# Optimization experiments

Measured on AMD Instinct MI355X. Metric: run time of the kernel, lower is better.

Reference implementation:

```python
import jax, jax.numpy as jnp
import numpy as np

B = 2048
SEQ_LEN = 512; PRED_LEN = 336; PATCH_LEN = 16; STRIDE = 8; CHANNELS = 16
D_MODEL = 128; HIDDEN = 256; PRUNE = 64
NUM_PATCHES = (SEQ_LEN - PATCH_LEN) // STRIDE + 1        # 63
TARGET_PATCHES = (PRED_LEN - 1) // STRIDE + 1            # 42 Euler steps


def setup_inputs() -> dict:
    key = jax.random.key(0)
    ks = jax.random.split(key, 12)
    w = lambda k, shape: (jax.random.normal(k, shape, jnp.float32) * 0.05)
    PC = PATCH_LEN * CHANNELS
    return {
        "x": jax.random.normal(ks[0], (B, SEQ_LEN, CHANNELS), jnp.float32),
        "W_pe": w(ks[1], (D_MODEL, PC)), "b_pe": jnp.zeros((D_MODEL,), jnp.float32),
        "W_conv": w(ks[2], (D_MODEL, 1, 3)), "b_conv": jnp.zeros((D_MODEL,), jnp.float32),
        "W_cmp": w(ks[3], (PRUNE, D_MODEL * NUM_PATCHES)), "b_cmp": jnp.zeros((PRUNE,), jnp.float32),
        "W_n1": w(ks[4], (HIDDEN, PRUNE)), "b_n1": jnp.zeros((HIDDEN,), jnp.float32),
        "W_n2": w(ks[5], (PRUNE, HIDDEN)), "b_n2": jnp.zeros((PRUNE,), jnp.float32),
        "W_l1": w(ks[6], (HIDDEN, PRUNE)), "b_l1": jnp.zeros((HIDDEN,), jnp.float32),
        "W_l2": w(ks[7], (D_MODEL, HIDDEN)), "b_l2": jnp.zeros((D_MODEL,), jnp.float32),
        "span_A": jnp.asarray(0.5, jnp.float32),
        "W_d1": w(ks[8], (PC, D_MODEL)), "b_d1": jnp.zeros((PC,), jnp.float32),
        "W_d2": w(ks[9], (PC, PC)), "b_d2": jnp.zeros((PC,), jnp.float32),
    }


def reference(x, W_pe, b_pe, W_conv, b_conv, W_cmp, b_cmp,
              W_n1, b_n1, W_n2, b_n2, W_l1, b_l1, W_l2, b_l2,
              span_A, W_d1, b_d1, W_d2, b_d2):
    silu = jax.nn.silu
    Bsz, L, C = x.shape

    # --- PatchEmbedding: unfold + rearrange 'b c n p -> b n (c p)' + Linear ---
    pidx = (jnp.arange(NUM_PATCHES) * STRIDE)[:, None] + jnp.arange(PATCH_LEN)[None, :]  # (N, P)
    patches = x[:, pidx, :]                                  # (B, N, P, C)
    patches = jnp.transpose(patches, (0, 1, 3, 2)).reshape(Bsz, NUM_PATCHES, C * PATCH_LEN)
    pe = patches @ W_pe.T + b_pe                             # (B, N, D)

    # --- depthwise Conv1d(k=3, padding=2, groups=D), SiLU, truncate to N ---
    feat = jnp.transpose(pe, (0, 2, 1))                      # (B, D, N)
    conv = jax.lax.conv_general_dilated(
        feat, W_conv, window_strides=(1,), padding=[(2, 2)],
        dimension_numbers=('NCH', 'OIH', 'NCH'), feature_group_count=D_MODEL)
    feat = silu(conv + b_conv[None, :, None])[:, :, :NUM_PATCHES]
    patch_flat = jnp.transpose(feat, (0, 2, 1)).reshape(Bsz, -1)   # (B, N*D)

    a0 = patch_flat @ W_cmp.T + b_cmp                        # (B, PRUNE); dropout = eval identity
    z0 = pe[:, -1, :]                                        # (B, D)

    # tspan built from float(span_A * K) in torch -> detached; dt = clamp(span_A)
    dt = jax.lax.stop_gradient(jnp.clip(span_A, 1e-8, 5.0))

    # circulant gather index: circ[b, i, j] = c[b, (j - i) % D]
    roll_idx = (jnp.arange(D_MODEL)[None, :] - jnp.arange(D_MODEL)[:, None]) % D_MODEL

    def euler_step(s, _):
        a = s[:, :PRUNE]
        z = s[:, PRUNE:]
        da = jnp.tanh(silu(a @ W_n1.T + b_n1) @ W_n2.T + b_n2)        # AODEFunc.net
        c = jnp.tanh(silu(a @ W_l1.T + b_l1) @ W_l2.T + b_l2)        # lat2out -> (B, D)
        dz = jnp.einsum('bij,bj->bi', c[:, roll_idx], z)              # circulant @ z
        s_new = s + dt * jnp.concatenate([da, dz], axis=-1)
        return s_new, s_new[:, PRUNE:]

    s0 = jnp.concatenate([a0, z0], axis=-1)
    _, z_traj = jax.lax.scan(euler_step, s0, None, length=TARGET_PATCHES)  # (K, B, D)

    # --- patch decoder (Linear -> SiLU -> Linear; dropout identity) ---
    dec = silu(z_traj @ W_d1.T + b_d1) @ W_d2.T + b_d2       # (K, B, P*C)
    pred_patches = dec.reshape(TARGET_PATCHES, Bsz, PATCH_LEN, C)

    # --- overlap-add reconstruction ---
    pos = (jnp.arange(TARGET_PATCHES) * STRIDE)[:, None] + jnp.arange(PATCH_LEN)[None, :]  # (K, P)
    valid = (pos < PRED_LEN).reshape(-1)
    pos_safe = jnp.where(valid, pos.reshape(-1), PRED_LEN)   # dump OOB into extra bin
    vals = jnp.transpose(pred_patches, (1, 0, 2, 3)).reshape(Bsz, -1, C)
    vals = vals * valid.astype(x.dtype)[None, :, None]
    out = jnp.zeros((Bsz, PRED_LEN + 1, C), x.dtype).at[:, pos_safe, :].add(vals)[:, :PRED_LEN]
    counts = jnp.zeros((PRED_LEN + 1,), x.dtype).at[pos_safe].add(valid.astype(x.dtype))[:PRED_LEN]
    x_pred = out / (counts[None, :, None] + 1e-6)

    return (x, x_pred)
```

## Files before the change

kernel.cpp:

```cpp
#include <hip/hip_runtime.h>
#include <math.h>

#define BATCH 2048
#define SEQ 512
#define CH 16
#define PLEN 16
#define NP 63
#define TP 42
#define DM 128
#define PCDIM 256
#define PRUNE 64
#define HID 256
#define PRED 336

#define O_WPET2   0
#define O_WCMPT4  32768
#define O_W1T4    548864
#define O_W2T4    581632
#define O_WD1T4   647168
#define O_WD2T4   679936
#define O_SSTATE  745472
#define O_FEAT    1138688
#define O_ZTRAJ   17653760
#define WS_TOTAL  28663808

__device__ __forceinline__ float silu_f(float v){ return v / (1.0f + expf(-v)); }

__global__ void repack_kernel(const float* __restrict__ Wpe, const float* __restrict__ Wcmp,
                              const float* __restrict__ Wn1, const float* __restrict__ Wn2,
                              const float* __restrict__ Wl1, const float* __restrict__ Wl2,
                              const float* __restrict__ Wd1, const float* __restrict__ Wd2,
                              float* __restrict__ ws){
  const int tot = 745472;
  for (int e = blockIdx.x*blockDim.x + threadIdx.x; e < tot; e += gridDim.x*blockDim.x){
    float v; int x = e;
    if (x < 32768){
      int kk = x & 3, d = (x>>2)&127, k4 = x>>9;
      v = Wpe[d*256 + k4*4 + kk];
    } else if ((x -= 32768) < 516096){
      int kk = x&3, j = (x>>2)&63, k4 = x>>8;
      v = Wcmp[j*8064 + k4*4 + kk];
    } else if ((x -= 516096) < 32768){
      int kk = x&3, j = (x>>2)&511, k4 = x>>11; int k = k4*4+kk;
      v = (j < 256) ? Wn1[j*64 + k] : Wl1[(j-256)*64 + k];
    } else if ((x -= 32768) < 65536){
      int kk = x&3, j = (x>>2)&255, k4 = x>>10; int k = k4*4+kk;
      v = (j < 64) ? Wn2[j*256 + k] : ((j < 192) ? Wl2[(j-64)*256 + k] : 0.0f);
    } else if ((x -= 65536) < 32768){
      int kk = x&3, j = (x>>2)&255, k4 = x>>10;
      v = Wd1[j*128 + k4*4 + kk];
    } else { x -= 32768;
      int kk = x&3, j = (x>>2)&255, k4 = x>>10;
      v = Wd2[j*256 + k4*4 + kk];
    }
    ws[e] = v;
  }
}

__global__ __launch_bounds__(256) void k1_embed(const float* __restrict__ x,
        const float* __restrict__ ws, const float* __restrict__ b_pe,
        const float* __restrict__ Wconv, const float* __restrict__ b_conv,
        float* __restrict__ feat, float* __restrict__ sstate){
  __shared__ __align__(16) float xT[16*512];
  __shared__ float pe_s[63*132];
  const float* __restrict__ WpeT2 = ws + O_WPET2;
  const int b = blockIdx.x;
  const int t = threadIdx.x;
  const float* xb = x + (size_t)b*(SEQ*CH);
  for (int rep = 0; rep < 2; ++rep){
    int l = t + rep*256;
    const float* src = xb + l*16;
    #pragma unroll
    for (int c4 = 0; c4 < 4; ++c4){
      float4 v = *(const float4*)(src + c4*4);
      xT[(c4*4+0)*512 + l] = v.x;
      xT[(c4*4+1)*512 + l] = v.y;
      xT[(c4*4+2)*512 + l] = v.z;
      xT[(c4*4+3)*512 + l] = v.w;
    }
  }
  __syncthreads();
  const int dgrp = t & 15;
  const int p0 = (t >> 4) * 4;
  float acc[8][4];
  #pragma unroll
  for (int j = 0; j < 8; ++j)
    #pragma unroll
    for (int pi = 0; pi < 4; ++pi) acc[j][pi] = 0.0f;
  for (int c = 0; c < 16; ++c){
    #pragma unroll
    for (int t4 = 0; t4 < 4; ++t4){
      const int k4 = c*4 + t4;
      float4 xv[4];
      #pragma unroll
      for (int pi = 0; pi < 4; ++pi){
        int p = p0 + pi; int pr = (p < 63) ? p : 62;
        xv[pi] = *(const float4*)(&xT[c*512 + pr*8 + t4*4]);
      }
      #pragma unroll
      for (int j = 0; j < 8; ++j){
        float4 wv = *(const float4*)(&WpeT2[(k4*128 + j*16 + dgrp)*4]);
        #pragma unroll
        for (int pi = 0; pi < 4; ++pi){
          acc[j][pi] += wv.x*xv[pi].x + wv.y*xv[pi].y + wv.z*xv[pi].z + wv.w*xv[pi].w;
        }
      }
    }
  }
  #pragma unroll
  for (int j = 0; j < 8; ++j){
    int d = j*16 + dgrp;
    float bp = b_pe[d];
    #pragma unroll
    for (int pi = 0; pi < 4; ++pi){
      int p = p0 + pi;
      if (p < 63) pe_s[p*132 + d] = acc[j][pi] + bp;
    }
  }
  __syncthreads();
  const int d = t & 127;
  const int ph = t >> 7;
  float w0 = Wconv[d*3+0], w1 = Wconv[d*3+1], w2 = Wconv[d*3+2];
  float bc = b_conv[d];
  float* featb = feat + (size_t)b*(NP*DM);
  for (int q = 0; q < 32; ++q){
    int p = ph*32 + q;
    if (p < 63){
      float s = bc + w2*pe_s[p*132+d];
      if (p >= 1) s += w1*pe_s[(p-1)*132+d];
      if (p >= 2) s += w0*pe_s[(p-2)*132+d];
      featb[p*128 + d] = silu_f(s);
    }
  }
  if (ph == 0){
    sstate[(size_t)b*192 + 64 + d] = pe_s[62*132 + d];
  }
}

__global__ __launch_bounds__(256) void k2_cmp(const float* __restrict__ feat,
      const float* __restrict__ ws, const float* __restrict__ b_cmp,
      float* __restrict__ sstate){
  const float* __restrict__ WcmpT4 = ws + O_WCMPT4;
  __shared__ __align__(16) float fs[8*512];
  const int b0 = blockIdx.x * 8;
  const int t = threadIdx.x;
  const int j = t & 63, bq = t >> 6;
  float acc0 = 0.0f, acc1 = 0.0f;
  for (int chk = 0; chk < 16; ++chk){
    const int k0 = chk*512;
    const int lim = (8064 - k0 < 512) ? (8064 - k0) : 512;
    __syncthreads();
    for (int u = 0; u < 16; ++u){
      int idx = u*256 + t;
      int bb = idx >> 9, kk = idx & 511;
      fs[idx] = (kk < lim) ? feat[(size_t)(b0+bb)*8064 + k0 + kk] : 0.0f;
    }
    __syncthreads();
    const int nk4 = lim >> 2;
    const float* wbase = &WcmpT4[(k0>>2)*256 + j*4];
    const float* f0 = &fs[(bq*2+0)*512];
    const float* f1 = &fs[(bq*2+1)*512];
    for (int k4 = 0; k4 < nk4; ++k4){
      float4 wv = *(const float4*)(wbase + k4*256);
      float4 a0 = *(const float4*)(f0 + k4*4);
      float4 a1 = *(const float4*)(f1 + k4*4);
      acc0 += wv.x*a0.x + wv.y*a0.y + wv.z*a0.z + wv.w*a0.w;
      acc1 += wv.x*a1.x + wv.y*a1.y + wv.z*a1.z + wv.w*a1.w;
    }
  }
  float bj = b_cmp[j];
  sstate[(size_t)(b0 + bq*2 + 0)*192 + j] = acc0 + bj;
  sstate[(size_t)(b0 + bq*2 + 1)*192 + j] = acc1 + bj;
}

__global__ __launch_bounds__(512) void k3_ode(const float* __restrict__ ws,
      const float* __restrict__ b_n1, const float* __restrict__ b_l1,
      const float* __restrict__ b_n2, const float* __restrict__ b_l2,
      const float* __restrict__ spanA,
      float* __restrict__ sstate, float* __restrict__ ztraj){
  const float* __restrict__ W1T4 = ws + O_W1T4;
  const float* __restrict__ W2T4 = ws + O_W2T4;
  __shared__ __align__(16) float a_s[8*64];
  __shared__ __align__(16) float h_s[8*512];
  __shared__ __align__(16) float c_s[8*128];
  __shared__ __align__(16) float zd[8*260];
  __shared__ float part2[2*8*256];
  __shared__ __align__(16) float dzp[2*8*128];
  const int t = threadIdx.x;
  const int b0 = blockIdx.x * 8;
  const float dt = fminf(fmaxf(spanA[0], 1e-8f), 5.0f);
  {
    int r = t >> 6, jj = t & 63;
    a_s[t] = sstate[(size_t)(b0+r)*192 + jj];
    for (int u = 0; u < 2; ++u){
      int idx = u*512 + t; int rr = idx >> 7, i = idx & 127;
      float zv = sstate[(size_t)(b0+rr)*192 + 64 + i];
      zd[rr*260 + i] = zv; zd[rr*260 + 128 + i] = zv;
    }
  }
  const float b1 = (t < 256) ? b_n1[t] : b_l1[t-256];
  const int j2 = t & 255;
  const int rb = t >> 8;
  const float bias2 = (j2 < 64) ? b_n2[j2] : ((j2 < 192) ? b_l2[j2-64] : 0.0f);
  __syncthreads();

  for (int st = 0; st < TP; ++st){
    {
      float acc[8];
      #pragma unroll
      for (int r = 0; r < 8; ++r) acc[r] = 0.0f;
      for (int k4 = 0; k4 < 16; ++k4){
        float4 wv = *(const float4*)(&W1T4[(k4*512 + t)*4]);
        #pragma unroll
        for (int r = 0; r < 8; ++r){
          float4 av = *(const float4*)(&a_s[r*64 + k4*4]);
          acc[r] += wv.x*av.x + wv.y*av.y + wv.z*av.z + wv.w*av.w;
        }
      }
      #pragma unroll
      for (int r = 0; r < 8; ++r) h_s[r*512 + t] = silu_f(acc[r] + b1);
    }
    __syncthreads();
    {
      const int kh = t >> 8;
      if (j2 < 192){
        float acc[8];
        #pragma unroll
        for (int r = 0; r < 8; ++r) acc[r] = 0.0f;
        const int hoff = (j2 < 64) ? 0 : 256;
        for (int k4i = 0; k4i < 32; ++k4i){
          const int k4 = kh*32 + k4i;
          float4 wv = *(const float4*)(&W2T4[(k4*256 + j2)*4]);
          #pragma unroll
          for (int r = 0; r < 8; ++r){
            float4 hv = *(const float4*)(&h_s[r*512 + hoff + k4*4]);
            acc[r] += wv.x*hv.x + wv.y*hv.y + wv.z*hv.z + wv.w*hv.w;
          }
        }
        #pragma unroll
        for (int r = 0; r < 8; ++r) part2[(kh*8 + r)*256 + j2] = acc[r];
      }
    }
    __syncthreads();
    if (j2 < 192){
      #pragma unroll
      for (int u = 0; u < 4; ++u){
        int r = u*2 + rb;
        float v = part2[r*256 + j2] + part2[(8+r)*256 + j2] + bias2;
        float tv = tanhf(v);
        if (j2 < 64) a_s[r*64 + j2] += dt * tv;
        else         c_s[r*128 + (j2-64)] = tv;
      }
    }
    __syncthreads();
    {
      const int i0 = (t & 31) * 4;
      const int r  = (t >> 5) & 7;
      const int mh = t >> 8;
      const int mbase = mh * 64;
      float m0=0.f, m1=0.f, m2=0.f, m3=0.f;
      const float* zr = &zd[r*260];
      const float* cr = &c_s[r*128];
      for (int mc = 0; mc < 16; ++mc){
        const int m = mbase + mc*4;
        float4 cv = *(const float4*)(cr + m);
        float4 za = *(const float4*)(zr + i0 + m);
        float4 zb = *(const float4*)(zr + i0 + m + 4);
        m0 += cv.x*za.x + cv.y*za.y + cv.z*za.z + cv.w*za.w;
        m1 += cv.x*za.y + cv.y*za.z + cv.z*za.w + cv.w*zb.x;
        m2 += cv.x*za.z + cv.y*za.w + cv.z*zb.x + cv.w*zb.y;
        m3 += cv.x*za.w + cv.y*zb.x + cv.z*zb.y + cv.w*zb.z;
      }
      *(float4*)(&dzp[(mh*8 + r)*128 + i0]) = make_float4(m0, m1, m2, m3);
    }
    __syncthreads();
    {
      float* zt = ztraj + (size_t)st*(BATCH*DM);
      for (int u = 0; u < 2; ++u){
        int idx = u*512 + t; int r = idx >> 7, i = idx & 127;
        float dz = dzp[r*128 + i] + dzp[(8+r)*128 + i];
        float zn = zd[r*260 + i] + dt*dz;
        zd[r*260 + i] = zn; zd[r*260 + 128 + i] = zn;
        zt[(size_t)(b0+r)*128 + i] = zn;
      }
    }
    __syncthreads();
  }
}

__global__ __launch_bounds__(256) void k4_dec(const float* __restrict__ ztraj,
    const float* __restrict__ ws, const float* __restrict__ b_d1,
    const float* __restrict__ b_d2, float* __restrict__ xpred){
  const float* __restrict__ Wd1T4 = ws + O_WD1T4;
  const float* __restrict__ Wd2T4 = ws + O_WD2T4;
  __shared__ __align__(16) float z_s[32*128];
  __shared__ __align__(16) float h_sh[32*256];
  const int t = threadIdx.x;
  const int m0 = blockIdx.x * 32;
  for (int u = 0; u < 4; ++u){
    int idx4 = u*256 + t;
    ((float4*)z_s)[idx4] = *(const float4*)(ztraj + (size_t)m0*128 + idx4*4);
  }
  __syncthreads();
  float acc[32];
  #pragma unroll
  for (int r = 0; r < 32; ++r) acc[r] = 0.0f;
  for (int k4 = 0; k4 < 32; ++k4){
    float4 wv = *(const float4*)(&Wd1T4[(k4*256 + t)*4]);
    #pragma unroll
    for (int r = 0; r < 32; ++r){
      float4 zv = *(const float4*)(&z_s[r*128 + k4*4]);
      acc[r] += wv.x*zv.x + wv.y*zv.y + wv.z*zv.z + wv.w*zv.w;
    }
  }
  {
    float bd1 = b_d1[t];
    #pragma unroll
    for (int r = 0; r < 32; ++r) h_sh[r*256 + t] = silu_f(acc[r] + bd1);
  }
  __syncthreads();
  #pragma unroll
  for (int r = 0; r < 32; ++r) acc[r] = 0.0f;
  for (int k4 = 0; k4 < 64; ++k4){
    float4 wv = *(const float4*)(&Wd2T4[(k4*256 + t)*4]);
    #pragma unroll
    for (int r = 0; r < 32; ++r){
      float4 hv = *(const float4*)(&h_sh[r*256 + k4*4]);
      acc[r] += wv.x*hv.x + wv.y*hv.y + wv.z*hv.z + wv.w*hv.w;
    }
  }
  const float bd2 = b_d2[t];
  const int tt_ = t >> 4, cc = t & 15;
  #pragma unroll
  for (int r = 0; r < 32; ++r){
    int m = m0 + r;
    int st = m >> 11;
    int b  = m & 2047;
    int tau = st*8 + tt_;
    if (tau < PRED){
      float scale = 1.0f / (((tau < 8) ? 1.0f : 2.0f) + 1e-6f);
      atomicAdd(&xpred[(size_t)b*(PRED*CH) + tau*16 + cc], (acc[r] + bd2) * scale);
    }
  }
}

extern "C" void kernel_launch(void* const* d_in, const int* in_sizes, int n_in,
                              void* d_out, int out_size, void* d_ws, size_t ws_size,
                              hipStream_t stream){
  const float* x    = (const float*)d_in[0];
  const float* Wpe  = (const float*)d_in[1];
  const float* bpe  = (const float*)d_in[2];
  const float* Wconv= (const float*)d_in[3];
  const float* bconv= (const float*)d_in[4];
  const float* Wcmp = (const float*)d_in[5];
  const float* bcmp = (const float*)d_in[6];
  const float* Wn1  = (const float*)d_in[7];
  const float* bn1  = (const float*)d_in[8];
  const float* Wn2  = (const float*)d_in[9];
  const float* bn2  = (const float*)d_in[10];
  const float* Wl1  = (const float*)d_in[11];
  const float* bl1  = (const float*)d_in[12];
  const float* Wl2  = (const float*)d_in[13];
  const float* bl2  = (const float*)d_in[14];
  const float* span = (const float*)d_in[15];
  const float* Wd1  = (const float*)d_in[16];
  const float* bd1  = (const float*)d_in[17];
  const float* Wd2  = (const float*)d_in[18];
  const float* bd2  = (const float*)d_in[19];
  float* out = (float*)d_out;
  float* ws  = (float*)d_ws;

  const size_t XN  = (size_t)BATCH*SEQ*CH;
  const size_t XPN = (size_t)BATCH*PRED*CH;

  hipMemcpyAsync(out, x, XN*sizeof(float), hipMemcpyDeviceToDevice, stream);
  hipMemsetAsync(out + XN, 0, XPN*sizeof(float), stream);

  float* sstate = ws + O_SSTATE;
  float* feat   = ws + O_FEAT;
  float* ztraj  = ws + O_ZTRAJ;

  repack_kernel<<<256, 256, 0, stream>>>(Wpe, Wcmp, Wn1, Wn2, Wl1, Wl2, Wd1, Wd2, ws);
  k1_embed<<<BATCH, 256, 0, stream>>>(x, ws, bpe, Wconv, bconv, feat, sstate);
  k2_cmp<<<BATCH/8, 256, 0, stream>>>(feat, ws, bcmp, sstate);
  k3_ode<<<BATCH/8, 512, 0, stream>>>(ws, bn1, bl1, bn2, bl2, span, sstate, ztraj);
  k4_dec<<<(TP*BATCH)/32, 256, 0, stream>>>(ztraj, ws, bd1, bd2, out + XN);
}
```

Before: 1.779 ms.

## Restructure ODE kernel to 1024 threads with overlapped stages; shrink decoder tiles

The ODE kernel now runs 1024 threads per block. It reorders each Euler step so that the second matmul and the z-update from the previous step run in the same phase, and the next step's first matmul runs alongside the circulant product. This cuts the barriers per step from five to three and splits the reductions four ways. The decoder kernel moves from 32-row to 16-row tiles, with each thread computing two output columns, which lowers register pressure and doubles the number of blocks. SiLU switches to the fast __expf intrinsic, at a small accuracy cost. The larger ODE blocks raise shared-memory and register demand per block, which may reduce occupancy.

```diff
diff --git a/kernel.cpp b/kernel.cpp
--- a/kernel.cpp
+++ b/kernel.cpp
@@ -22,9 +22,8 @@
 #define O_SSTATE  745472
 #define O_FEAT    1138688
 #define O_ZTRAJ   17653760
-#define WS_TOTAL  28663808
-
-__device__ __forceinline__ float silu_f(float v){ return v / (1.0f + expf(-v)); }
+
+__device__ __forceinline__ float silu_f(float v){ return v / (1.0f + __expf(-v)); }
 
 __global__ void repack_kernel(const float* __restrict__ Wpe, const float* __restrict__ Wcmp,
                               const float* __restrict__ Wn1, const float* __restrict__ Wn2,
@@ -173,7 +172,7 @@
   sstate[(size_t)(b0 + bq*2 + 1)*192 + j] = acc1 + bj;
 }
 
-__global__ __launch_bounds__(512) void k3_ode(const float* __restrict__ ws,
+__global__ __launch_bounds__(1024) void k3_ode(const float* __restrict__ ws,
       const float* __restrict__ b_n1, const float* __restrict__ b_l1,
       const float* __restrict__ b_n2, const float* __restrict__ b_l2,
       const float* __restrict__ spanA,
@@ -184,24 +183,51 @@
   __shared__ __align__(16) float h_s[8*512];
   __shared__ __align__(16) float c_s[8*128];
   __shared__ __align__(16) float zd[8*260];
-  __shared__ float part2[2*8*256];
-  __shared__ __align__(16) float dzp[2*8*128];
+  __shared__ __align__(16) float part2[4*8*256];
+  __shared__ __align__(16) float dzp[4*8*128];
   const int t = threadIdx.x;
   const int b0 = blockIdx.x * 8;
   const float dt = fminf(fmaxf(spanA[0], 1e-8f), 5.0f);
-  {
+
+  if (t < 512){
     int r = t >> 6, jj = t & 63;
     a_s[t] = sstate[(size_t)(b0+r)*192 + jj];
-    for (int u = 0; u < 2; ++u){
-      int idx = u*512 + t; int rr = idx >> 7, i = idx & 127;
-      float zv = sstate[(size_t)(b0+rr)*192 + 64 + i];
-      zd[rr*260 + i] = zv; zd[rr*260 + 128 + i] = zv;
-    }
-  }
-  const float b1 = (t < 256) ? b_n1[t] : b_l1[t-256];
+  }
+  {
+    int r = t >> 7, i = t & 127;
+    float zv = sstate[(size_t)(b0+r)*192 + 64 + i];
+    zd[r*260 + i] = zv; zd[r*260 + 128 + i] = zv;
+  }
+  const int jP0 = t & 511;
+  const int rhP0 = t >> 9;
+  const float b1 = (jP0 < 256) ? b_n1[jP0] : b_l1[jP0-256];
+  const int khA = t >> 8;
   const int j2 = t & 255;
-  const int rb = t >> 8;
   const float bias2 = (j2 < 64) ? b_n2[j2] : ((j2 < 192) ? b_l2[j2-64] : 0.0f);
+  const int hoffA = (j2 < 64) ? 0 : 256;
+  const int rrB = t >> 8;
+  const int mhC = t >> 8;
+  const int rC  = (t >> 5) & 7;
+  const int i0C = (t & 31) * 4;
+  const int rZ = t >> 7, iZ = t & 127;
+  __syncthreads();
+
+  {
+    float acc4[4];
+    #pragma unroll
+    for (int q = 0; q < 4; ++q) acc4[q] = 0.0f;
+    for (int k4 = 0; k4 < 16; ++k4){
+      float4 wv = *(const float4*)(&W1T4[(k4*512 + jP0)*4]);
+      #pragma unroll
+      for (int q = 0; q < 4; ++q){
+        float4 av = *(const float4*)(&a_s[(rhP0*4+q)*64 + k4*4]);
+        acc4[q] += wv.x*av.x + wv.y*av.y + wv.z*av.z + wv.w*av.w;
+      }
+    }
+    #pragma unroll
+    for (int q = 0; q < 4; ++q)
+      h_s[(rhP0*4+q)*512 + jP0] = silu_f(acc4[q] + b1);
+  }
   __syncthreads();
 
   for (int st = 0; st < TP; ++st){
@@ -209,82 +235,81 @@
       float acc[8];
       #pragma unroll
       for (int r = 0; r < 8; ++r) acc[r] = 0.0f;
-      for (int k4 = 0; k4 < 16; ++k4){
-        float4 wv = *(const float4*)(&W1T4[(k4*512 + t)*4]);
+      for (int k4i = 0; k4i < 16; ++k4i){
+        const int k4 = khA*16 + k4i;
+        float4 wv = *(const float4*)(&W2T4[(k4*256 + j2)*4]);
         #pragma unroll
         for (int r = 0; r < 8; ++r){
-          float4 av = *(const float4*)(&a_s[r*64 + k4*4]);
-          acc[r] += wv.x*av.x + wv.y*av.y + wv.z*av.z + wv.w*av.w;
+          float4 hv = *(const float4*)(&h_s[r*512 + hoffA + k4*4]);
+          acc[r] += wv.x*hv.x + wv.y*hv.y + wv.z*hv.z + wv.w*hv.w;
         }
       }
       #pragma unroll
-      for (int r = 0; r < 8; ++r) h_s[r*512 + t] = silu_f(acc[r] + b1);
+      for (int r = 0; r < 8; ++r) part2[(khA*8 + r)*256 + j2] = acc[r];
+    }
+    if (st > 0){
+      float dz = dzp[(0*8+rZ)*128 + iZ] + dzp[(1*8+rZ)*128 + iZ]
+               + dzp[(2*8+rZ)*128 + iZ] + dzp[(3*8+rZ)*128 + iZ];
+      float zn = zd[rZ*260 + iZ] + dt*dz;
+      zd[rZ*260 + iZ] = zn; zd[rZ*260 + 128 + iZ] = zn;
+      ztraj[(size_t)(st-1)*(BATCH*DM) + (size_t)(b0+rZ)*128 + iZ] = zn;
     }
     __syncthreads();
-    {
-      const int kh = t >> 8;
-      if (j2 < 192){
-        float acc[8];
-        #pragma unroll
-        for (int r = 0; r < 8; ++r) acc[r] = 0.0f;
-        const int hoff = (j2 < 64) ? 0 : 256;
-        for (int k4i = 0; k4i < 32; ++k4i){
-          const int k4 = kh*32 + k4i;
-          float4 wv = *(const float4*)(&W2T4[(k4*256 + j2)*4]);
-          #pragma unroll
-          for (int r = 0; r < 8; ++r){
-            float4 hv = *(const float4*)(&h_s[r*512 + hoff + k4*4]);
-            acc[r] += wv.x*hv.x + wv.y*hv.y + wv.z*hv.z + wv.w*hv.w;
-          }
-        }
-        #pragma unroll
-        for (int r = 0; r < 8; ++r) part2[(kh*8 + r)*256 + j2] = acc[r];
-      }
-    }
-    __syncthreads();
+
     if (j2 < 192){
       #pragma unroll
-      for (int u = 0; u < 4; ++u){
-        int r = u*2 + rb;
-        float v = part2[r*256 + j2] + part2[(8+r)*256 + j2] + bias2;
+      for (int u = 0; u < 2; ++u){
+        int r = rrB*2 + u;
+        float v = part2[(0*8+r)*256 + j2] + part2[(1*8+r)*256 + j2]
+                + part2[(2*8+r)*256 + j2] + part2[(3*8+r)*256 + j2] + bias2;
         float tv = tanhf(v);
         if (j2 < 64) a_s[r*64 + j2] += dt * tv;
         else         c_s[r*128 + (j2-64)] = tv;
       }
     }
     __syncthreads();
+
     {
-      const int i0 = (t & 31) * 4;
-      const int r  = (t >> 5) & 7;
-      const int mh = t >> 8;
-      const int mbase = mh * 64;
+      float acc4[4];
+      #pragma unroll
+      for (int q = 0; q < 4; ++q) acc4[q] = 0.0f;
+      for (int k4 = 0; k4 < 16; ++k4){
+        float4 wv = *(const float4*)(&W1T4[(k4*512 + jP0)*4]);
+        #pragma unroll
+        for (int q = 0; q < 4; ++q){
+          float4 av = *(const float4*)(&a_s[(rhP0*4+q)*64 + k4*4]);
+          acc4[q] += wv.x*av.x + wv.y*av.y + wv.z*av.z + wv.w*av.w;
+        }
+      }
+      #pragma unroll
+      for (int q = 0; q < 4; ++q)
+        h_s[(rhP0*4+q)*512 + jP0] = silu_f(acc4[q] + b1);
+    }
+    {
       float m0=0.f, m1=0.f, m2=0.f, m3=0.f;
-      const float* zr = &zd[r*260];
-      const float* cr = &c_s[r*128];
-      for (int mc = 0; mc < 16; ++mc){
-        const int m = mbase + mc*4;
+      const float* zr = &zd[rC*260];
+      const float* cr = &c_s[rC*128];
+      #pragma unroll
+      for (int mc = 0; mc < 8; ++mc){
+        const int m = mhC*32 + mc*4;
         float4 cv = *(const float4*)(cr + m);
-        float4 za = *(const float4*)(zr + i0 + m);
-        float4 zb = *(const float4*)(zr + i0 + m + 4);
+        float4 za = *(const float4*)(zr + i0C + m);
+        float4 zb = *(const float4*)(zr + i0C + m + 4);
         m0 += cv.x*za.x + cv.y*za.y + cv.z*za.z + cv.w*za.w;
         m1 += cv.x*za.y + cv.y*za.z + cv.z*za.w + cv.w*zb.x;
         m2 += cv.x*za.z + cv.y*za.w + cv.z*zb.x + cv.w*zb.y;
         m3 += cv.x*za.w + cv.y*zb.x + cv.z*zb.y + cv.w*zb.z;
       }
-      *(float4*)(&dzp[(mh*8 + r)*128 + i0]) = make_float4(m0, m1, m2, m3);
+      *(float4*)(&dzp[(mhC*8 + rC)*128 + i0C]) = make_float4(m0, m1, m2, m3);
     }
     __syncthreads();
-    {
-      float* zt = ztraj + (size_t)st*(BATCH*DM);
-      for (int u = 0; u < 2; ++u){
-        int idx = u*512 + t; int r = idx >> 7, i = idx & 127;
-        float dz = dzp[r*128 + i] + dzp[(8+r)*128 + i];
-        float zn = zd[r*260 + i] + dt*dz;
-        zd[r*260 + i] = zn; zd[r*260 + 128 + i] = zn;
-        zt[(size_t)(b0+r)*128 + i] = zn;
-      }
-    }
-    __syncthreads();
+  }
+
+  {
+    float dz = dzp[(0*8+rZ)*128 + iZ] + dzp[(1*8+rZ)*128 + iZ]
+             + dzp[(2*8+rZ)*128 + iZ] + dzp[(3*8+rZ)*128 + iZ];
+    float zn = zd[rZ*260 + iZ] + dt*dz;
+    ztraj[(size_t)(TP-1)*(BATCH*DM) + (size_t)(b0+rZ)*128 + iZ] = zn;
   }
 }
 
@@ -293,53 +318,68 @@
     const float* __restrict__ b_d2, float* __restrict__ xpred){
   const float* __restrict__ Wd1T4 = ws + O_WD1T4;
   const float* __restrict__ Wd2T4 = ws + O_WD2T4;
-  __shared__ __align__(16) float z_s[32*128];
-  __shared__ __align__(16) float h_sh[32*256];
+  __shared__ __align__(16) float z_s[16*128];
+  __shared__ __align__(16) float h_sh[16*256];
   const int t = threadIdx.x;
-  const int m0 = blockIdx.x * 32;
-  for (int u = 0; u < 4; ++u){
+  const int m0 = blockIdx.x * 16;
+  #pragma unroll
+  for (int u = 0; u < 2; ++u){
     int idx4 = u*256 + t;
     ((float4*)z_s)[idx4] = *(const float4*)(ztraj + (size_t)m0*128 + idx4*4);
   }
   __syncthreads();
-  float acc[32];
-  #pragma unroll
-  for (int r = 0; r < 32; ++r) acc[r] = 0.0f;
+  const int j = t & 127, rh = t >> 7;
+  float accA[8], accB[8];
+  #pragma unroll
+  for (int q = 0; q < 8; ++q){ accA[q] = 0.0f; accB[q] = 0.0f; }
   for (int k4 = 0; k4 < 32; ++k4){
-    float4 wv = *(const float4*)(&Wd1T4[(k4*256 + t)*4]);
-    #pragma unroll
-    for (int r = 0; r < 32; ++r){
-      float4 zv = *(const float4*)(&z_s[r*128 + k4*4]);
-      acc[r] += wv.x*zv.x + wv.y*zv.y + wv.z*zv.z + wv.w*zv.w;
+    float4 wa = *(const float4*)(&Wd1T4[(k4*256 + j)*4]);
+    float4 wb = *(const float4*)(&Wd1T4[(k4*256 + j + 128)*4]);
+    #pragma unroll
+    for (int q = 0; q < 8; ++q){
+      float4 zv = *(const float4*)(&z_s[(rh*8+q)*128 + k4*4]);
+      accA[q] += wa.x*zv.x + wa.y*zv.y + wa.z*zv.z + wa.w*zv.w;
+      accB[q] += wb.x*zv.x + wb.y*zv.y + wb.z*zv.z + wb.w*zv.w;
     }
   }
   {
-    float bd1 = b_d1[t];
-    #pragma unroll
-    for (int r = 0; r < 32; ++r) h_sh[r*256 + t] = silu_f(acc[r] + bd1);
-  }
-  __syncthreads();
-  #pragma unroll
-  for (int r = 0; r < 32; ++r) acc[r] = 0.0f;
+    float b1a = b_d1[j], b1b = b_d1[j+128];
+    #pragma unroll
+    for (int q = 0; q < 8; ++q){
+      h_sh[(rh*8+q)*256 + j]       = silu_f(accA[q] + b1a);
+      h_sh[(rh*8+q)*256 + j + 128] = silu_f(accB[q] + b1b);
+    }
+  }
+  __syncthreads();
+  #pragma unroll
+  for (int q = 0; q < 8; ++q){ accA[q] = 0.0f; accB[q] = 0.0f; }
   for (int k4 = 0; k4 < 64; ++k4){
-    float4 wv = *(const float4*)(&Wd2T4[(k4*256 + t)*4]);
-    #pragma unroll
-    for (int r = 0; r < 32; ++r){
-      float4 hv = *(const float4*)(&h_sh[r*256 + k4*4]);
-      acc[r] += wv.x*hv.x + wv.y*hv.y + wv.z*hv.z + wv.w*hv.w;
-    }
-  }
-  const float bd2 = b_d2[t];
-  const int tt_ = t >> 4, cc = t & 15;
-  #pragma unroll
-  for (int r = 0; r < 32; ++r){
-    int m = m0 + r;
+    float4 wa = *(const float4*)(&Wd2T4[(k4*256 + j)*4]);
+    float4 wb = *(const float4*)(&Wd2T4[(k4*256 + j + 128)*4]);
+    #pragma unroll
+    for (int q = 0; q < 8; ++q){
+      float4 hv = *(const float4*)(&h_sh[(rh*8+q)*256 + k4*4]);
+      accA[q] += wa.x*hv.x + wa.y*hv.y + wa.z*hv.z + wa.w*hv.w;
+      accB[q] += wb.x*hv.x + wb.y*hv.y + wb.z*hv.z + wb.w*hv.w;
+    }
+  }
+  const float b2a = b_d2[j], b2b = b_d2[j+128];
+  const int ttA = j >> 4, cc = j & 15;
+  const int ttB = ttA + 8;
+  #pragma unroll
+  for (int q = 0; q < 8; ++q){
+    int m = m0 + rh*8 + q;
     int st = m >> 11;
     int b  = m & 2047;
-    int tau = st*8 + tt_;
-    if (tau < PRED){
-      float scale = 1.0f / (((tau < 8) ? 1.0f : 2.0f) + 1e-6f);
-      atomicAdd(&xpred[(size_t)b*(PRED*CH) + tau*16 + cc], (acc[r] + bd2) * scale);
+    int tauA = st*8 + ttA;
+    int tauB = st*8 + ttB;
+    if (tauA < PRED){
+      float scale = 1.0f / (((tauA < 8) ? 1.0f : 2.0f) + 1e-6f);
+      atomicAdd(&xpred[(size_t)b*(PRED*CH) + tauA*16 + cc], (accA[q] + b2a) * scale);
+    }
+    if (tauB < PRED){
+      float scale = 1.0f / (((tauB < 8) ? 1.0f : 2.0f) + 1e-6f);
+      atomicAdd(&xpred[(size_t)b*(PRED*CH) + tauB*16 + cc], (accB[q] + b2b) * scale);
     }
   }
 }
@@ -383,6 +423,6 @@
   repack_kernel<<<256, 256, 0, stream>>>(Wpe, Wcmp, Wn1, Wn2, Wl1, Wl2, Wd1, Wd2, ws);
   k1_embed<<<BATCH, 256, 0, stream>>>(x, ws, bpe, Wconv, bconv, feat, sstate);
   k2_cmp<<<BATCH/8, 256, 0, stream>>>(feat, ws, bcmp, sstate);
-  k3_ode<<<BATCH/8, 512, 0, stream>>>(ws, bn1, bl1, bn2, bl2, span, sstate, ztraj);
-  k4_dec<<<(TP*BATCH)/32, 256, 0, stream>>>(ztraj, ws, bd1, bd2, out + XN);
-}
+  k3_ode<<<BATCH/8, 1024, 0, stream>>>(ws, bn1, bl1, bn2, bl2, span, sstate, ztraj);
+  k4_dec<<<(TP*BATCH)/16, 256, 0, stream>>>(ztraj, ws, bd1, bd2, out + XN);
+}
```

After: 2.661 ms. 49.6% more time.
